# Optimization experiments

Hardware: AMD Instinct MI355X
Metric: run time of the kernel (lower is better)

## Reference

```python
import jax, jax.numpy as jnp
import numpy as np
import math

S, W, H = 256, 128, 768   # sentence, word, hidden (hidden fixed to 768 by PositionalEncoding)
TOPK = 3                  # len(inputs) > 2 branch: fuse 3 nearest sentences


def positional_encoding(length, d_model):
    # Standard sinusoidal PE, identical to the torch buffer construction.
    pos = jnp.arange(length, dtype=jnp.float32)[:, None]                      # [L,1]
    div = jnp.exp(jnp.arange(0, d_model, 2, dtype=jnp.float32)
                  * (-math.log(10000.0) / d_model))                           # [H/2]
    pe = jnp.zeros((length, d_model), dtype=jnp.float32)
    pe = pe.at[:, 0::2].set(jnp.sin(pos * div))
    pe = pe.at[:, 1::2].set(jnp.cos(pos * div))
    return pe


def setup_inputs() -> dict:
    key = jax.random.key(0)
    inputs = jax.random.normal(key, (S, W, H), dtype=jnp.float32)
    return {"inputs": inputs}


def reference(inputs):
    s, w, h = inputs.shape
    # Pairwise L1 distance between the FIRST word vector of each sentence
    # (matmulCell only ever sees x[i,0,:] and k[0,j,:] == inputs[j,0,:]).
    x0 = inputs[:, 0, :]                                                      # [S,H]
    dist = jnp.sum(jnp.abs(x0[:, None, :] - x0[None, :, :]), axis=-1)         # [S,S]
    # torch.sort ascending -> 3 nearest sentences (self included, dist 0)
    idx = jnp.argsort(dist, axis=1)[:, :TOPK]                                 # [S,3] int
    fused = inputs[idx].reshape(s, TOPK * w, h)                               # [S,3W,H]
    # Positional encoding added to both q/v stream and k stream (same tensor;
    # dropout p=0.1 is identity in eval mode).
    x = fused + positional_encoding(TOPK * w, h)[None]                        # [S,3W,H]
    # Scaled dot-product self-attention per row.
    scores = jnp.einsum('slh,smh->slm', x, x) / jnp.sqrt(jnp.float32(h))      # [S,3W,3W]
    attn = jax.nn.softmax(scores, axis=-1)
    out = jnp.einsum('slm,smh->slh', attn, x)                                 # [S,3W,H]
    # D_Attention keeps only the first word-1 rows of each fused output.
    return out[:, :w - 1, :]                                                  # [S,W-1,H]
```

## Files before the change

kernel.cpp:

```cpp
#include <hip/hip_runtime.h>

#define NS 256
#define NW 128
#define NH 768
#define NL 384
#define WH (NW*NH)
#define OUTROWS 127

typedef __attribute__((ext_vector_type(8))) short short8;
typedef __attribute__((ext_vector_type(8))) unsigned short ushort8;
typedef __attribute__((ext_vector_type(8))) __bf16 bf16x8;
typedef __attribute__((ext_vector_type(4))) float f32x4;

#define XS2_STRIDE 136
#define PS_STRIDE 392
#define SMEM_PS   55296
#define SMEM_RED  (SMEM_PS + 128*PS_STRIDE*2)
#define SMEM_TOTAL (SMEM_RED + 4096)

__device__ __forceinline__ unsigned short bf16b(float f) {
  union { float f; unsigned u; } x; x.f = f;
  return (unsigned short)((x.u + 0x7fffu + ((x.u >> 16) & 1u)) >> 16);
}
__device__ __forceinline__ float b2f(unsigned short h) {
  union { unsigned u; float f; } x; x.u = ((unsigned)h) << 16;
  return x.f;
}
__device__ __forceinline__ unsigned short bfc(float f) {
  __bf16 h = (__bf16)f;
  return __builtin_bit_cast(unsigned short, h);
}

__global__ __launch_bounds__(1024) void k_pre(const float* __restrict__ inp,
                                              int* __restrict__ idxw,
                                              unsigned short* __restrict__ peb,
                                              unsigned short* __restrict__ inpb) {
  const int t = threadIdx.x;
  const int b = blockIdx.x;
  if (b >= 544) {
    size_t base = ((size_t)(b - 544) * 1024 + t) * 8;
    float4 a = *(const float4*)(inp + base);
    float4 c = *(const float4*)(inp + base + 4);
    ushort8 o;
    o[0] = bfc(a.x); o[1] = bfc(a.y); o[2] = bfc(a.z); o[3] = bfc(a.w);
    o[4] = bfc(c.x); o[5] = bfc(c.y); o[6] = bfc(c.z); o[7] = bfc(c.w);
    *(ushort8*)(inpb + base) = o;
    return;
  }
  if (b >= NS) {
    int gid = (b - NS) * 1024 + t;
    int l = gid / NH, d = gid - l * NH;
    const float c = -0.011992630687355995f;
    float dv = __expf((float)(d & ~1) * c);
    float ang = (float)l * dv;
    float v = (d & 1) ? cosf(ang) : sinf(ang);
    peb[gid] = bf16b(v);
    return;
  }
  const int i = b;
  __shared__ float xi[772];
  __shared__ float dist[NS];
  __shared__ unsigned long long wkeys[16];
  for (int h = t; h < NH; h += 1024) xi[h + h / 192] = inp[(size_t)i * WH + h];
  __syncthreads();
  const int c = t >> 2, seg = t & 3;
  const float* __restrict__ row = inp + (size_t)c * WH + seg * 192;
  const float* xis = xi + seg * 193;
  float s = 0.f;
  #pragma unroll 4
  for (int h = 0; h < 192; h += 4) {
    float4 v = *(const float4*)(row + h);
    s += fabsf(xis[h]     - v.x) + fabsf(xis[h + 1] - v.y)
       + fabsf(xis[h + 2] - v.z) + fabsf(xis[h + 3] - v.w);
  }
  s += __shfl_xor(s, 1, 64);
  s += __shfl_xor(s, 2, 64);
  if (seg == 0) dist[c] = s;
  __syncthreads();
  for (int k = 0; k < 3; ++k) {
    float d = (t < NS) ? dist[t] : 3.4e38f;
    unsigned long long key = ((unsigned long long)__float_as_uint(d) << 32) | (unsigned)t;
    #pragma unroll
    for (int dd = 1; dd < 64; dd <<= 1) {
      unsigned long long o = __shfl_xor(key, dd, 64);
      key = (o < key) ? o : key;
    }
    if ((t & 63) == 0) wkeys[t >> 6] = key;
    __syncthreads();
    if (t == 0) {
      unsigned long long best = wkeys[0];
      for (int w = 1; w < 16; ++w) if (wkeys[w] < best) best = wkeys[w];
      int bj = (int)(best & 0xffffffffu);
      idxw[i * 3 + k] = bj;
      dist[bj] = 3.4e38f;
    }
    __syncthreads();
  }
}

__global__ __launch_bounds__(512)
void k_attn(const unsigned short* __restrict__ inpb, const unsigned short* __restrict__ peb,
            const int* __restrict__ idxw, float* __restrict__ out) {
  extern __shared__ char smem[];
  unsigned short* Xs = (unsigned short*)smem;
  unsigned short* Ps = (unsigned short*)(smem + SMEM_PS);
  float* red1 = (float*)(smem + SMEM_RED);
  float* red2 = red1 + 512;

  const int s = blockIdx.x;
  const int tid = threadIdx.x;
  const int lane = tid & 63, wid = tid >> 6;
  const int lrow = lane & 15, lhi = lane >> 4;
  const int i0 = idxw[s * 3 + 0], i1 = idxw[s * 3 + 1], i2 = idxw[s * 3 + 2];

  const f32x4 fz = {0.f, 0.f, 0.f, 0.f};
  f32x4 acc[4][6];
  #pragma unroll
  for (int qs = 0; qs < 4; ++qs)
    #pragma unroll
    for (int kf = 0; kf < 6; ++kf) acc[qs][kf] = fz;

  const int qh = wid & 1, kq = wid >> 1;

  for (int hc = 0; hc < 6; ++hc) {
    const int h0 = hc * 128;
    #pragma unroll
    for (int it = 0; it < 12; ++it) {
      const int src = (it < 4) ? i0 : (it < 8 ? i1 : i2);
      const int rls = (it & 3) * 32 + (tid >> 4);
      const int r   = it * 32 + (tid >> 4);
      const int cc  = (tid & 15) * 8;
      ushort8 xv = *(const ushort8*)&inpb[(size_t)src * WH + (size_t)rls * NH + h0 + cc];
      ushort8 pv = *(const ushort8*)&peb[r * NH + h0 + cc];
      bf16x8 o;
      #pragma unroll
      for (int j = 0; j < 8; ++j) o[j] = (__bf16)(b2f(xv[j]) + b2f(pv[j]));
      *reinterpret_cast<bf16x8*>(&Xs[r * XS2_STRIDE + cc]) = o;
    }
    __syncthreads();
    __builtin_amdgcn_s_setprio(1);
    #pragma unroll
    for (int ks = 0; ks < 128; ks += 32) {
      short8 a[4];
      #pragma unroll
      for (int qs = 0; qs < 4; ++qs)
        a[qs] = *reinterpret_cast<const short8*>(&Xs[(qh * 64 + qs * 16 + lrow) * XS2_STRIDE + ks + lhi * 8]);
      #pragma unroll
      for (int kf = 0; kf < 6; ++kf) {
        short8 b = *reinterpret_cast<const short8*>(&Xs[(kq * 96 + kf * 16 + lrow) * XS2_STRIDE + ks + lhi * 8]);
        #pragma unroll
        for (int qs = 0; qs < 4; ++qs)
          acc[qs][kf] = __builtin_amdgcn_mfma_f32_16x16x32_bf16(a[qs], b, acc[qs][kf], 0, 0, 0);
      }
    }
    __builtin_amdgcn_s_setprio(0);
    __syncthreads();
  }

  const float scale = 0.03608439182435161f;
  float mx[4][4];
  #pragma unroll
  for (int qs = 0; qs < 4; ++qs)
    #pragma unroll
    for (int r = 0; r < 4; ++r) {
      float m = acc[qs][0][r];
      #pragma unroll
      for (int kf = 1; kf < 6; ++kf) m = fmaxf(m, acc[qs][kf][r]);
      #pragma unroll
      for (int d = 1; d < 16; d <<= 1) m = fmaxf(m, __shfl_xor(m, d, 64));
      mx[qs][r] = m;
    }
  if (lrow == 0) {
    #pragma unroll
    for (int qs = 0; qs < 4; ++qs)
      #pragma unroll
      for (int r = 0; r < 4; ++r)
        red1[(qh * 64 + qs * 16 + lhi * 4 + r) * 4 + kq] = mx[qs][r];
  }
  __syncthreads();
  float sm[4][4];
  #pragma unroll
  for (int qs = 0; qs < 4; ++qs)
    #pragma unroll
    for (int r = 0; r < 4; ++r) {
      const int row = qh * 64 + qs * 16 + lhi * 4 + r;
      float4 m0 = *(const float4*)&red1[row * 4];
      mx[qs][r] = fmaxf(fmaxf(m0.x, m0.y), fmaxf(m0.z, m0.w));
      sm[qs][r] = 0.f;
    }
  #pragma unroll
  for (int qs = 0; qs < 4; ++qs)
    #pragma unroll
    for (int kf = 0; kf < 6; ++kf)
      #pragma unroll
      for (int r = 0; r < 4; ++r) {
        float p = __expf((acc[qs][kf][r] - mx[qs][r]) * scale);
        acc[qs][kf][r] = p;
        sm[qs][r] += p;
      }
  #pragma unroll
  for (int qs = 0; qs < 4; ++qs)
    #pragma unroll
    for (int r = 0; r < 4; ++r) {
      #pragma unroll
      for (int d = 1; d < 16; d <<= 1) sm[qs][r] += __shfl_xor(sm[qs][r], d, 64);
    }
  if (lrow == 0) {
    #pragma unroll
    for (int qs = 0; qs < 4; ++qs)
      #pragma unroll
      for (int r = 0; r < 4; ++r)
        red2[(qh * 64 + qs * 16 + lhi * 4 + r) * 4 + kq] = sm[qs][r];
  }
  __syncthreads();
  #pragma unroll
  for (int qs = 0; qs < 4; ++qs)
    #pragma unroll
    for (int r = 0; r < 4; ++r) {
      const int row = qh * 64 + qs * 16 + lhi * 4 + r;
      float4 s0 = *(const float4*)&red2[row * 4];
      sm[qs][r] = 1.0f / ((s0.x + s0.y) + (s0.z + s0.w));
    }
  #pragma unroll
  for (int qs = 0; qs < 4; ++qs)
    #pragma unroll
    for (int kf = 0; kf < 6; ++kf)
      #pragma unroll
      for (int r = 0; r < 4; ++r) {
        const int row = qh * 64 + qs * 16 + lhi * 4 + r;
        const int col = kq * 96 + kf * 16 + lrow;
        *(unsigned short*)((char*)Ps + (((row * PS_STRIDE + col) * 2) ^ (((row >> 3) & 7) << 4))) =
            bfc(acc[qs][kf][r] * sm[qs][r]);
      }
  __syncthreads();

  const int qb = wid & 3, hh = wid >> 2;
  short8 pa[2][12];
  #pragma unroll
  for (int qs = 0; qs < 2; ++qs)
    #pragma unroll
    for (int m0 = 0; m0 < 12; ++m0) {
      const int row = qb * 32 + qs * 16 + lrow;
      pa[qs][m0] = *reinterpret_cast<const short8*>(
          (const char*)Ps + (((row * PS_STRIDE + m0 * 32 + lhi * 8) * 2) ^ (((row >> 3) & 7) << 4)));
    }

  unsigned short* VT = Xs;
  const int rl0 = tid >> 3, c8 = (tid & 7) * 8;
  for (int t4 = 0; t4 < 12; ++t4) {
    const int h0 = t4 * 64;
    #pragma unroll
    for (int it = 0; it < 6; ++it) {
      const int src = (it < 2) ? i0 : (it < 4 ? i1 : i2);
      const int ml = rl0 + (it & 1) * 64;
      const int m  = ml + (it >> 1) * 128;
      ushort8 xv = *(const ushort8*)&inpb[(size_t)src * WH + (size_t)ml * NH + h0 + c8];
      ushort8 pv = *(const ushort8*)&peb[m * NH + h0 + c8];
      #pragma unroll
      for (int j = 0; j < 8; ++j) {
        const int vr = c8 + j;
        VT[((vr * PS_STRIDE) + m) ^ (((vr >> 3) & 7) << 3)] = bfc(b2f(xv[j]) + b2f(pv[j]));
      }
    }
    __syncthreads();
    __builtin_amdgcn_s_setprio(1);
    f32x4 o00 = fz, o01 = fz, o10 = fz, o11 = fz;
    const int vr0 = hh * 32 + lrow, vr1 = vr0 + 16;
    const int sw0 = ((vr0 >> 3) & 7) << 4, sw1 = ((vr1 >> 3) & 7) << 4;
    #pragma unroll
    for (int mm = 0; mm < 12; ++mm) {
      const int moff = (mm * 32 + lhi * 8) * 2;
      short8 b0 = *reinterpret_cast<const short8*>((const char*)VT + ((vr0 * PS_STRIDE * 2 + moff) ^ sw0));
      short8 b1 = *reinterpret_cast<const short8*>((const char*)VT + ((vr1 * PS_STRIDE * 2 + moff) ^ sw1));
      o00 = __builtin_amdgcn_mfma_f32_16x16x32_bf16(pa[0][mm], b0, o00, 0, 0, 0);
      o01 = __builtin_amdgcn_mfma_f32_16x16x32_bf16(pa[0][mm], b1, o01, 0, 0, 0);
      o10 = __builtin_amdgcn_mfma_f32_16x16x32_bf16(pa[1][mm], b0, o10, 0, 0, 0);
      o11 = __builtin_amdgcn_mfma_f32_16x16x32_bf16(pa[1][mm], b1, o11, 0, 0, 0);
    }
    __builtin_amdgcn_s_setprio(0);
    float* ob = out + (size_t)s * (OUTROWS * NH) + h0 + hh * 32 + lrow;
    #pragma unroll
    for (int qs = 0; qs < 2; ++qs)
      #pragma unroll
      for (int hf = 0; hf < 2; ++hf) {
        f32x4 o = (qs == 0) ? (hf == 0 ? o00 : o01) : (hf == 0 ? o10 : o11);
        #pragma unroll
        for (int r = 0; r < 4; ++r) {
          const int q = qb * 32 + qs * 16 + lhi * 4 + r;
          if (q < OUTROWS) ob[(size_t)q * NH + hf * 16] = o[r];
        }
      }
    __syncthreads();
  }
}

extern "C" void kernel_launch(void* const* d_in, const int* in_sizes, int n_in,
                              void* d_out, int out_size, void* d_ws, size_t ws_size,
                              hipStream_t stream) {
  (void)in_sizes; (void)n_in; (void)out_size; (void)ws_size;
  const float* inp = (const float*)d_in[0];
  float* out = (float*)d_out;
  char* ws = (char*)d_ws;

  unsigned short* peb = (unsigned short*)ws;
  int* idxw           = (int*)(ws + 589824);
  unsigned short* inpb= (unsigned short*)(ws + 592896);

  hipLaunchKernelGGL(k_pre, dim3(256 + 288 + 3072), dim3(1024), 0, stream,
                     inp, idxw, peb, inpb);

  hipFuncSetAttribute((const void*)k_attn,
                      hipFuncAttributeMaxDynamicSharedMemorySize, SMEM_TOTAL);
  hipLaunchKernelGGL(k_attn, dim3(256), dim3(512), SMEM_TOTAL, stream,
                     inpb, peb, idxw, out);
}
```

Baseline: 127.7 us.

## Precompute PE-added bf16 slabs and double-buffer QK tiles via global_load_lds

A new pre-pass writes three bf16 copies of the input, one per slab position, with the positional encoding already added. This lets the attention kernel skip the per-block PE add and conversion work. The QK^T phase now streams 64-wide hidden chunks straight into LDS with global_load_lds into two swizzled buffers, so the next chunk loads while MFMAs run on the current one. This needs about 150MB of workspace and triples the bf16 write traffic of the pre-pass, and a fallback path keeps the old kernels for when the workspace is too small.

```diff
diff --git a/kernel.cpp b/kernel.cpp
--- a/kernel.cpp
+++ b/kernel.cpp
@@ -12,11 +12,18 @@
 typedef __attribute__((ext_vector_type(8))) __bf16 bf16x8;
 typedef __attribute__((ext_vector_type(4))) float f32x4;
 
+#define AS1(p) ((const __attribute__((address_space(1))) void*)(p))
+#define AS3(p) ((__attribute__((address_space(3))) void*)(p))
+
+#define QKBUF   49152
+#define PS_STRIDE 392
+#define OFF_RED 100352
+#define OFF_VT  104448
+#define SMEM_PRI 154624
 #define XS2_STRIDE 136
-#define PS_STRIDE 392
-#define SMEM_PS   55296
-#define SMEM_RED  (SMEM_PS + 128*PS_STRIDE*2)
-#define SMEM_TOTAL (SMEM_RED + 4096)
+#define FB_SMEM_PS   55296
+#define FB_SMEM_RED  (FB_SMEM_PS + 128*PS_STRIDE*2)
+#define FB_SMEM_TOTAL (FB_SMEM_RED + 4096)
 
 __device__ __forceinline__ unsigned short bf16b(float f) {
   union { float f; unsigned u; } x; x.f = f;
@@ -31,22 +38,11 @@
   return __builtin_bit_cast(unsigned short, h);
 }
 
-__global__ __launch_bounds__(1024) void k_pre(const float* __restrict__ inp,
-                                              int* __restrict__ idxw,
-                                              unsigned short* __restrict__ peb,
-                                              unsigned short* __restrict__ inpb) {
+__global__ __launch_bounds__(1024) void k_pre1(const float* __restrict__ inp,
+                                               int* __restrict__ idxw,
+                                               unsigned short* __restrict__ peb) {
   const int t = threadIdx.x;
   const int b = blockIdx.x;
-  if (b >= 544) {
-    size_t base = ((size_t)(b - 544) * 1024 + t) * 8;
-    float4 a = *(const float4*)(inp + base);
-    float4 c = *(const float4*)(inp + base + 4);
-    ushort8 o;
-    o[0] = bfc(a.x); o[1] = bfc(a.y); o[2] = bfc(a.z); o[3] = bfc(a.w);
-    o[4] = bfc(c.x); o[5] = bfc(c.y); o[6] = bfc(c.z); o[7] = bfc(c.w);
-    *(ushort8*)(inpb + base) = o;
-    return;
-  }
   if (b >= NS) {
     int gid = (b - NS) * 1024 + t;
     int l = gid / NH, d = gid - l * NH;
@@ -98,13 +94,252 @@
   }
 }
 
+__global__ __launch_bounds__(1024) void k_pc3(const float* __restrict__ inp,
+                                              const unsigned short* __restrict__ peb,
+                                              unsigned short* __restrict__ xpe) {
+  const size_t gid = (size_t)blockIdx.x * 1024 + threadIdx.x;
+  const int row = (int)(gid / 96);
+  const int w8  = (int)(gid - (size_t)row * 96) * 8;
+  const int slab = row >> 15, src = (row >> 7) & 255, rl = row & 127;
+  const float* px = inp + ((size_t)src * 128 + rl) * NH + w8;
+  float4 a = *(const float4*)px;
+  float4 b = *(const float4*)(px + 4);
+  ushort8 pv = *(const ushort8*)&peb[(slab * 128 + rl) * NH + w8];
+  ushort8 o;
+  o[0] = bfc(a.x + b2f(pv[0])); o[1] = bfc(a.y + b2f(pv[1]));
+  o[2] = bfc(a.z + b2f(pv[2])); o[3] = bfc(a.w + b2f(pv[3]));
+  o[4] = bfc(b.x + b2f(pv[4])); o[5] = bfc(b.y + b2f(pv[5]));
+  o[6] = bfc(b.z + b2f(pv[6])); o[7] = bfc(b.w + b2f(pv[7]));
+  *(ushort8*)(xpe + gid * 8) = o;
+}
+
+__global__ __launch_bounds__(1024) void k_pre_fb(const float* __restrict__ inp,
+                                                 unsigned short* __restrict__ inpb) {
+  size_t base = ((size_t)blockIdx.x * 1024 + threadIdx.x) * 8;
+  float4 a = *(const float4*)(inp + base);
+  float4 c = *(const float4*)(inp + base + 4);
+  ushort8 o;
+  o[0] = bfc(a.x); o[1] = bfc(a.y); o[2] = bfc(a.z); o[3] = bfc(a.w);
+  o[4] = bfc(c.x); o[5] = bfc(c.y); o[6] = bfc(c.z); o[7] = bfc(c.w);
+  *(ushort8*)(inpb + base) = o;
+}
+
 __global__ __launch_bounds__(512)
-void k_attn(const unsigned short* __restrict__ inpb, const unsigned short* __restrict__ peb,
-            const int* __restrict__ idxw, float* __restrict__ out) {
+void k_attn(const unsigned short* __restrict__ xpe, const int* __restrict__ idxw,
+            float* __restrict__ out) {
+  extern __shared__ char smem[];
+  unsigned short* Ps = (unsigned short*)smem;
+  float* red1 = (float*)(smem + OFF_RED);
+  float* red2 = red1 + 512;
+  unsigned short* VT = (unsigned short*)(smem + OFF_VT);
+
+  const int s = blockIdx.x;
+  const int tid = threadIdx.x;
+  const int lane = tid & 63, wid = tid >> 6;
+  const int lrow = lane & 15, lhi = lane >> 4;
+  int idx3[3];
+  idx3[0] = idxw[s * 3 + 0]; idx3[1] = idxw[s * 3 + 1]; idx3[2] = idxw[s * 3 + 2];
+
+  const f32x4 fz = {0.f, 0.f, 0.f, 0.f};
+  f32x4 acc[4][6];
+  #pragma unroll
+  for (int qs = 0; qs < 4; ++qs)
+    #pragma unroll
+    for (int kf = 0; kf < 6; ++kf) acc[qs][kf] = fz;
+
+  const int qh = wid & 1, kq = wid >> 1;
+  const int irow0 = wid * 48;
+  const int lr8 = lane >> 3, lslot = lane & 7;
+
+  auto issue = [&](int buf, int h0) {
+    #pragma unroll
+    for (int i = 0; i < 6; ++i) {
+      const int row = irow0 + i * 8 + lr8;
+      const int slab = row >> 7, rl = row & 127;
+      const int cg = lslot ^ (row & 7);
+      const unsigned short* g = xpe +
+          (((size_t)slab * 256 + idx3[slab]) * 128 + rl) * (size_t)NH + h0 + cg * 8;
+      __builtin_amdgcn_global_load_lds(AS1(g), AS3(smem + buf * QKBUF + (irow0 + i * 8) * 128),
+                                       16, 0, 0);
+    }
+  };
+
+  issue(0, 0);
+  for (int hc = 0; hc < 12; ++hc) {
+    const int cur = hc & 1;
+    if (hc < 11) {
+      issue(cur ^ 1, (hc + 1) * 64);
+      asm volatile("s_waitcnt vmcnt(6)" ::: "memory");
+    } else {
+      asm volatile("s_waitcnt vmcnt(0)" ::: "memory");
+    }
+    __builtin_amdgcn_s_barrier();
+    const unsigned short* Xc = (const unsigned short*)(smem + cur * QKBUF);
+    __builtin_amdgcn_s_setprio(1);
+    #pragma unroll
+    for (int ks = 0; ks < 64; ks += 32) {
+      short8 a[4];
+      #pragma unroll
+      for (int qs = 0; qs < 4; ++qs) {
+        const int ar = qh * 64 + qs * 16 + lrow;
+        a[qs] = *reinterpret_cast<const short8*>(
+            &Xc[ar * 64 + ((((ks >> 3) + lhi) ^ (ar & 7)) << 3)]);
+      }
+      #pragma unroll
+      for (int kf = 0; kf < 6; ++kf) {
+        const int br = kq * 96 + kf * 16 + lrow;
+        short8 b = *reinterpret_cast<const short8*>(
+            &Xc[br * 64 + ((((ks >> 3) + lhi) ^ (br & 7)) << 3)]);
+        #pragma unroll
+        for (int qs = 0; qs < 4; ++qs)
+          acc[qs][kf] = __builtin_amdgcn_mfma_f32_16x16x32_bf16(a[qs], b, acc[qs][kf], 0, 0, 0);
+      }
+    }
+    __builtin_amdgcn_s_setprio(0);
+    __builtin_amdgcn_s_barrier();
+  }
+
+  const float scale = 0.03608439182435161f;
+  float mx[4][4];
+  #pragma unroll
+  for (int qs = 0; qs < 4; ++qs)
+    #pragma unroll
+    for (int r = 0; r < 4; ++r) {
+      float m = acc[qs][0][r];
+      #pragma unroll
+      for (int kf = 1; kf < 6; ++kf) m = fmaxf(m, acc[qs][kf][r]);
+      #pragma unroll
+      for (int d = 1; d < 16; d <<= 1) m = fmaxf(m, __shfl_xor(m, d, 64));
+      mx[qs][r] = m;
+    }
+  if (lrow == 0) {
+    #pragma unroll
+    for (int qs = 0; qs < 4; ++qs)
+      #pragma unroll
+      for (int r = 0; r < 4; ++r)
+        red1[(qh * 64 + qs * 16 + lhi * 4 + r) * 4 + kq] = mx[qs][r];
+  }
+  __syncthreads();
+  float sm[4][4];
+  #pragma unroll
+  for (int qs = 0; qs < 4; ++qs)
+    #pragma unroll
+    for (int r = 0; r < 4; ++r) {
+      const int row = qh * 64 + qs * 16 + lhi * 4 + r;
+      float4 m0 = *(const float4*)&red1[row * 4];
+      mx[qs][r] = fmaxf(fmaxf(m0.x, m0.y), fmaxf(m0.z, m0.w));
+      sm[qs][r] = 0.f;
+    }
+  #pragma unroll
+  for (int qs = 0; qs < 4; ++qs)
+    #pragma unroll
+    for (int kf = 0; kf < 6; ++kf)
+      #pragma unroll
+      for (int r = 0; r < 4; ++r) {
+        float p = __expf((acc[qs][kf][r] - mx[qs][r]) * scale);
+        acc[qs][kf][r] = p;
+        sm[qs][r] += p;
+      }
+  #pragma unroll
+  for (int qs = 0; qs < 4; ++qs)
+    #pragma unroll
+    for (int r = 0; r < 4; ++r) {
+      #pragma unroll
+      for (int d = 1; d < 16; d <<= 1) sm[qs][r] += __shfl_xor(sm[qs][r], d, 64);
+    }
+  if (lrow == 0) {
+    #pragma unroll
+    for (int qs = 0; qs < 4; ++qs)
+      #pragma unroll
+      for (int r = 0; r < 4; ++r)
+        red2[(qh * 64 + qs * 16 + lhi * 4 + r) * 4 + kq] = sm[qs][r];
+  }
+  __syncthreads();
+  #pragma unroll
+  for (int qs = 0; qs < 4; ++qs)
+    #pragma unroll
+    for (int r = 0; r < 4; ++r) {
+      const int row = qh * 64 + qs * 16 + lhi * 4 + r;
+      float4 s0 = *(const float4*)&red2[row * 4];
+      sm[qs][r] = 1.0f / ((s0.x + s0.y) + (s0.z + s0.w));
+    }
+  #pragma unroll
+  for (int qs = 0; qs < 4; ++qs)
+    #pragma unroll
+    for (int kf = 0; kf < 6; ++kf)
+      #pragma unroll
+      for (int r = 0; r < 4; ++r) {
+        const int row = qh * 64 + qs * 16 + lhi * 4 + r;
+        const int col = kq * 96 + kf * 16 + lrow;
+        *(unsigned short*)((char*)Ps + (((row * PS_STRIDE + col) * 2) ^ (((row >> 3) & 7) << 4))) =
+            bfc(acc[qs][kf][r] * sm[qs][r]);
+      }
+  __syncthreads();
+
+  const int qb = wid & 3, hh = wid >> 2;
+  short8 pa[2][12];
+  #pragma unroll
+  for (int qs = 0; qs < 2; ++qs)
+    #pragma unroll
+    for (int m0 = 0; m0 < 12; ++m0) {
+      const int row = qb * 32 + qs * 16 + lrow;
+      pa[qs][m0] = *reinterpret_cast<const short8*>(
+          (const char*)Ps + (((row * PS_STRIDE + m0 * 32 + lhi * 8) * 2) ^ (((row >> 3) & 7) << 4)));
+    }
+  const int rl0 = tid >> 3, c8 = (tid & 7) * 8;
+  for (int t4 = 0; t4 < 12; ++t4) {
+    const int h0 = t4 * 64;
+    #pragma unroll
+    for (int it = 0; it < 6; ++it) {
+      const int slab = it >> 1;
+      const int ml = rl0 + (it & 1) * 64;
+      const int m  = ml + slab * 128;
+      ushort8 xv = *(const ushort8*)&xpe[(((size_t)slab * 256 + idx3[slab]) * 128 + ml) * (size_t)NH + h0 + c8];
+      #pragma unroll
+      for (int j = 0; j < 8; ++j) {
+        const int vr = c8 + j;
+        VT[((vr * PS_STRIDE) + m) ^ (((vr >> 3) & 7) << 3)] = xv[j];
+      }
+    }
+    __syncthreads();
+    __builtin_amdgcn_s_setprio(1);
+    f32x4 o00 = fz, o01 = fz, o10 = fz, o11 = fz;
+    const int vr0 = hh * 32 + lrow, vr1 = vr0 + 16;
+    const int sw0 = ((vr0 >> 3) & 7) << 4, sw1 = ((vr1 >> 3) & 7) << 4;
+    #pragma unroll
+    for (int mm = 0; mm < 12; ++mm) {
+      const int moff = (mm * 32 + lhi * 8) * 2;
+      short8 b0 = *reinterpret_cast<const short8*>((const char*)VT + ((vr0 * PS_STRIDE * 2 + moff) ^ sw0));
+      short8 b1 = *reinterpret_cast<const short8*>((const char*)VT + ((vr1 * PS_STRIDE * 2 + moff) ^ sw1));
+      o00 = __builtin_amdgcn_mfma_f32_16x16x32_bf16(pa[0][mm], b0, o00, 0, 0, 0);
+      o01 = __builtin_amdgcn_mfma_f32_16x16x32_bf16(pa[0][mm], b1, o01, 0, 0, 0);
+      o10 = __builtin_amdgcn_mfma_f32_16x16x32_bf16(pa[1][mm], b0, o10, 0, 0, 0);
+      o11 = __builtin_amdgcn_mfma_f32_16x16x32_bf16(pa[1][mm], b1, o11, 0, 0, 0);
+    }
+    __builtin_amdgcn_s_setprio(0);
+    float* ob = out + (size_t)s * (OUTROWS * NH) + h0 + hh * 32 + lrow;
+    #pragma unroll
+    for (int qs = 0; qs < 2; ++qs)
+      #pragma unroll
+      for (int hf = 0; hf < 2; ++hf) {
+        f32x4 o = (qs == 0) ? (hf == 0 ? o00 : o01) : (hf == 0 ? o10 : o11);
+        #pragma unroll
+        for (int r = 0; r < 4; ++r) {
+          const int q = qb * 32 + qs * 16 + lhi * 4 + r;
+          if (q < OUTROWS) ob[(size_t)q * NH + hf * 16] = o[r];
+        }
+      }
+    __syncthreads();
+  }
+}
+
+__global__ __launch_bounds__(512)
+void k_attn_fb(const unsigned short* __restrict__ inpb, const unsigned short* __restrict__ peb,
+               const int* __restrict__ idxw, float* __restrict__ out) {
   extern __shared__ char smem[];
   unsigned short* Xs = (unsigned short*)smem;
-  unsigned short* Ps = (unsigned short*)(smem + SMEM_PS);
-  float* red1 = (float*)(smem + SMEM_RED);
+  unsigned short* Ps = (unsigned short*)(smem + FB_SMEM_PS);
+  float* red1 = (float*)(smem + FB_SMEM_RED);
   float* red2 = red1 + 512;
 
   const int s = blockIdx.x;
@@ -121,7 +356,6 @@
     for (int kf = 0; kf < 6; ++kf) acc[qs][kf] = fz;
 
   const int qh = wid & 1, kq = wid >> 1;
-
   for (int hc = 0; hc < 6; ++hc) {
     const int h0 = hc * 128;
     #pragma unroll
@@ -156,7 +390,6 @@
     __builtin_amdgcn_s_setprio(0);
     __syncthreads();
   }
-
   const float scale = 0.03608439182435161f;
   float mx[4][4];
   #pragma unroll
@@ -233,7 +466,6 @@
             bfc(acc[qs][kf][r] * sm[qs][r]);
       }
   __syncthreads();
-
   const int qb = wid & 3, hh = wid >> 2;
   short8 pa[2][12];
   #pragma unroll
@@ -244,7 +476,6 @@
       pa[qs][m0] = *reinterpret_cast<const short8*>(
           (const char*)Ps + (((row * PS_STRIDE + m0 * 32 + lhi * 8) * 2) ^ (((row >> 3) & 7) << 4)));
     }
-
   unsigned short* VT = Xs;
   const int rl0 = tid >> 3, c8 = (tid & 7) * 8;
   for (int t4 = 0; t4 < 12; ++t4) {
@@ -297,20 +528,28 @@
 extern "C" void kernel_launch(void* const* d_in, const int* in_sizes, int n_in,
                               void* d_out, int out_size, void* d_ws, size_t ws_size,
                               hipStream_t stream) {
-  (void)in_sizes; (void)n_in; (void)out_size; (void)ws_size;
+  (void)in_sizes; (void)n_in; (void)out_size;
   const float* inp = (const float*)d_in[0];
   float* out = (float*)d_out;
   char* ws = (char*)d_ws;
 
   unsigned short* peb = (unsigned short*)ws;
   int* idxw           = (int*)(ws + 589824);
-  unsigned short* inpb= (unsigned short*)(ws + 592896);
-
-  hipLaunchKernelGGL(k_pre, dim3(256 + 288 + 3072), dim3(1024), 0, stream,
-                     inp, idxw, peb, inpb);
-
-  hipFuncSetAttribute((const void*)k_attn,
-                      hipFuncAttributeMaxDynamicSharedMemorySize, SMEM_TOTAL);
-  hipLaunchKernelGGL(k_attn, dim3(256), dim3(512), SMEM_TOTAL, stream,
-                     inpb, peb, idxw, out);
-}
+  unsigned short* big = (unsigned short*)(ws + 592896);
+  const bool primary = ws_size >= (size_t)592896 + (size_t)150994944;
+
+  hipLaunchKernelGGL(k_pre1, dim3(544), dim3(1024), 0, stream, inp, idxw, peb);
+
+  if (primary) {
+    hipLaunchKernelGGL(k_pc3, dim3(9216), dim3(1024), 0, stream, inp, peb, big);
+    hipFuncSetAttribute((const void*)k_attn,
+                        hipFuncAttributeMaxDynamicSharedMemorySize, SMEM_PRI);
+    hipLaunchKernelGGL(k_attn, dim3(256), dim3(512), SMEM_PRI, stream, big, idxw, out);
+  } else {
+    hipLaunchKernelGGL(k_pre_fb, dim3(3072), dim3(1024), 0, stream, inp, big);
+    hipFuncSetAttribute((const void*)k_attn_fb,
+                        hipFuncAttributeMaxDynamicSharedMemorySize, FB_SMEM_TOTAL);
+    hipLaunchKernelGGL(k_attn_fb, dim3(256), dim3(512), FB_SMEM_TOTAL, stream,
+                       big, peb, idxw, out);
+  }
+}
```

New measurement: 160.5 us. +25.7%, slower.
